# Kernel tuning notes

Measured on AMD Instinct MI355X. Metric: run time of the kernel, lower is better.

## Reference

```python
import jax, jax.numpy as jnp
import numpy as np

C = 256
C8 = C // 8

def setup_inputs() -> dict:
    key = jax.random.key(0)
    ks = jax.random.split(key, 8)
    a = jax.random.normal(ks[0], (4, C, 64, 64), dtype=jnp.float32)
    s = 1.0 / np.sqrt(C)
    b_w = jax.random.normal(ks[1], (C8, C), dtype=jnp.float32) * s
    b_b = jnp.zeros((C8,), dtype=jnp.float32)
    c_w = jax.random.normal(ks[2], (C8, C), dtype=jnp.float32) * s
    c_b = jnp.zeros((C8,), dtype=jnp.float32)
    d_w = jax.random.normal(ks[3], (C, C), dtype=jnp.float32) * s
    d_b = jnp.zeros((C,), dtype=jnp.float32)
    alpha = jnp.zeros((1,), dtype=jnp.float32) + 0.5  # nonzero so attention path is exercised
    return {"a": a, "b_w": b_w, "b_b": b_b, "c_w": c_w, "c_b": c_b, "d_w": d_w, "d_b": d_b, "alpha": alpha}

def _conv1x1(x, w, b):
    # x: [n, c, h, w], w: [o, c] -> [n, o, h, w]
    return jnp.einsum('nchw,oc->nohw', x, w) + b[None, :, None, None]

def reference(a, b_w, b_b, c_w, c_b, d_w, d_b, alpha):
    n, chan, h, w = a.shape
    nhw = h * w
    b = _conv1x1(a, b_w, b_b).reshape(n, -1, nhw)   # [n, C/8, nhw]
    c = _conv1x1(a, c_w, c_b).reshape(n, -1, nhw)   # [n, C/8, nhw]
    k = jnp.einsum('nci,ncj->nij', b, c)            # [n, nhw, nhw]
    s = jax.nn.softmax(k, axis=-1)
    d = _conv1x1(a, d_w, d_b).reshape(n, -1, nhw)   # [n, C, nhw]
    kl = jnp.einsum('ncj,nij->nci', d, s)           # d @ s^T
    kl = kl.reshape(n, chan, h, w)
    return alpha * kl + a
```

## Files before the change

kernel.cpp:

```cpp
#include <hip/hip_runtime.h>
#include <hip/hip_bf16.h>

#define CCH 256
#define CQK 32
#define NHW 4096

typedef float f32x4 __attribute__((ext_vector_type(4)));
typedef _Float16 hv8 __attribute__((ext_vector_type(8)));
typedef _Float16 hv4 __attribute__((ext_vector_type(4)));
typedef __fp16 fv2 __attribute__((ext_vector_type(2)));

__device__ __forceinline__ unsigned enc_f32(float f) {
    unsigned u = __float_as_uint(f);
    return (u & 0x80000000u) ? ~u : (u | 0x80000000u);
}
__device__ __forceinline__ float dec_f32(unsigned u) {
    return __uint_as_float((u & 0x80000000u) ? (u ^ 0x80000000u) : ~u);
}

__global__ __launch_bounds__(256) void prep_kernel(
    const float* __restrict__ b_w, const float* __restrict__ c_w,
    const float* __restrict__ d_w, _Float16* __restrict__ Wh,
    unsigned* __restrict__ m_enc)
{
    const int bid = blockIdx.x, tid = threadIdx.x;
    if (bid < 80) {
        const int idx = (bid * 256 + tid) * 4;
        const int row = idx >> 8, col = idx & 255;
        const float* src = (row < 32) ? (b_w + row * CCH + col)
                         : (row < 64) ? (c_w + (row - 32) * CCH + col)
                                      : (d_w + (row - 64) * CCH + col);
        const float scl = (row < 32) ? 1.4426950408889634f : 1.0f;
        float4 v = *reinterpret_cast<const float4*>(src);
        _Float16* dst = Wh + (size_t)row * CCH + col;
        dst[0] = (_Float16)(v.x * scl); dst[1] = (_Float16)(v.y * scl);
        dst[2] = (_Float16)(v.z * scl); dst[3] = (_Float16)(v.w * scl);
    } else {
        m_enc[(bid - 80) * 256 + tid] = 0u;
    }
}

__global__ __launch_bounds__(256) void proj_kernel(
    const float* __restrict__ a, const _Float16* __restrict__ Wh,
    const float* __restrict__ b_b, const float* __restrict__ c_b,
    const float* __restrict__ d_b,
    _Float16* __restrict__ bqT, _Float16* __restrict__ ckT,
    _Float16* __restrict__ dv)
{
    __shared__ _Float16 aT[32][CCH + 24];

    const int n    = blockIdx.x >> 7;
    const int i0   = (blockIdx.x & 127) << 5;
    const int tid  = threadIdx.x;
    const int lane = tid & 63;
    const int wave = tid >> 6;
    const int l15  = lane & 15;
    const int quad = lane >> 4;

    {
        const float* ap = a + (size_t)(n*CCH + tid)*NHW + i0;
        #pragma unroll
        for (int j = 0; j < 8; ++j) {
            float4 v = *reinterpret_cast<const float4*>(ap + j*4);
            aT[j*4+0][tid] = (_Float16)v.x;
            aT[j*4+1][tid] = (_Float16)v.y;
            aT[j*4+2][tid] = (_Float16)v.z;
            aT[j*4+3][tid] = (_Float16)v.w;
        }
    }
    __syncthreads();

    const f32x4 zf = {0.f, 0.f, 0.f, 0.f};
    f32x4 acc[5][2];
    #pragma unroll
    for (int t = 0; t < 5; ++t) { acc[t][0] = zf; acc[t][1] = zf; }

    const int ch0w = wave * 80;

    #pragma unroll
    for (int ks = 0; ks < 8; ++ks) {
        const int k0 = ks * 32;
        hv8 af0 = *reinterpret_cast<const hv8*>(&aT[l15][k0 + quad*8]);
        hv8 af1 = *reinterpret_cast<const hv8*>(&aT[16 + l15][k0 + quad*8]);
        #pragma unroll
        for (int t = 0; t < 5; ++t) {
            const int ch0 = ch0w + t*16;
            hv8 bf = *reinterpret_cast<const hv8*>(
                Wh + (size_t)(ch0 + l15)*CCH + k0 + quad*8);
            acc[t][0] = __builtin_amdgcn_mfma_f32_16x16x32_f16(af0, bf, acc[t][0], 0, 0, 0);
            acc[t][1] = __builtin_amdgcn_mfma_f32_16x16x32_f16(af1, bf, acc[t][1], 0, 0, 0);
        }
    }

    const int pos_b = i0 + quad*4;
    #pragma unroll
    for (int t = 0; t < 5; ++t) {
        const int ch0 = ch0w + t*16;
        if (ch0 < 64) {
            const float* bias_arr = (ch0 < 32) ? b_b : c_b;
            _Float16*    outp     = (ch0 < 32) ? bqT : ckT;
            const int    ch       = (ch0 & 31) + l15;
            const float  bias     = bias_arr[ch] *
                ((ch0 < 32) ? 1.4426950408889634f : 1.0f);
            #pragma unroll
            for (int nf = 0; nf < 2; ++nf) {
                #pragma unroll
                for (int r = 0; r < 4; ++r) {
                    const int pos = pos_b + nf*16 + r;
                    outp[((size_t)n*NHW + pos)*CQK + ch] =
                        (_Float16)(acc[t][nf][r] + bias);
                }
            }
        } else {
            const int ch   = ch0 - 64 + l15;
            const float bias = d_b[ch];
            #pragma unroll
            for (int nf = 0; nf < 2; ++nf) {
                hv4 v = { (_Float16)(acc[t][nf][0] + bias),
                          (_Float16)(acc[t][nf][1] + bias),
                          (_Float16)(acc[t][nf][2] + bias),
                          (_Float16)(acc[t][nf][3] + bias) };
                *reinterpret_cast<hv4*>(
                    dv + ((size_t)n*CCH + ch)*NHW + pos_b + nf*16) = v;
            }
        }
    }
}

__global__ __launch_bounds__(256) void rowmax_kernel(
    const _Float16* __restrict__ bqT, const _Float16* __restrict__ ckT,
    unsigned* __restrict__ m_enc)
{
    const int bx   = blockIdx.x;
    const int n    = bx >> 8;
    const int qt   = (bx >> 2) & 63;
    const int ks   = bx & 3;
    const int q0   = qt << 6;
    const int tid  = threadIdx.x;
    const int wave = tid >> 6;
    const int lane = tid & 63;
    const int l15  = lane & 15;
    const int quad = lane >> 4;

    const f32x4 zf = {0.f, 0.f, 0.f, 0.f};
    const hv8 qf = *reinterpret_cast<const hv8*>(
        bqT + ((size_t)n*NHW + q0 + wave*16 + l15)*CQK + quad*8);

    float mx = -1e30f;

    for (int kt = ks*16; kt < ks*16 + 16; ++kt) {
        const int k0 = kt << 6;
        #pragma unroll
        for (int f = 0; f < 4; ++f) {
            hv8 kf = *reinterpret_cast<const hv8*>(
                ckT + ((size_t)n*NHW + k0 + f*16 + l15)*CQK + quad*8);
            f32x4 s = __builtin_amdgcn_mfma_f32_16x16x32_f16(kf, qf, zf, 0, 0, 0);
            mx = fmaxf(mx, fmaxf(fmaxf(s[0], s[1]), fmaxf(s[2], s[3])));
        }
    }
    mx = fmaxf(mx, __shfl_xor(mx, 16, 64));
    mx = fmaxf(mx, __shfl_xor(mx, 32, 64));
    if (lane < 16)
        atomicMax(&m_enc[n*NHW + q0 + wave*16 + l15], enc_f32(mx));
}

__global__ __launch_bounds__(256) void attn_kernel(
    const _Float16* __restrict__ bqT, const _Float16* __restrict__ ckT,
    const _Float16* __restrict__ dv, const unsigned* __restrict__ m_enc,
    const float* __restrict__ a, const float* __restrict__ alpha_p,
    float* __restrict__ out)
{
    __shared__ _Float16 dv_lds[2][128 * 72];
    __shared__ _Float16 p_lds[2][4][16 * 72];

    const int bx   = ((blockIdx.x & 7) << 6) | (blockIdx.x >> 3);
    const int n    = bx >> 7;
    const int cg   = (bx >> 6) & 1;
    const int q0   = (bx & 63) << 6;
    const int co0  = cg << 7;
    const int tid  = threadIdx.x;
    const int wave = tid >> 6;
    const int lane = tid & 63;
    const int l15  = lane & 15;
    const int quad = lane >> 4;

    const _Float16 one_h = (_Float16)1.0f;
    const hv8 ones = { one_h, one_h, one_h, one_h, one_h, one_h, one_h, one_h };

    const hv8 qf = *reinterpret_cast<const hv8*>(
        bqT + ((size_t)n*NHW + q0 + wave*16 + l15)*CQK + quad*8);

    const float mneg = -dec_f32(m_enc[n*NHW + q0 + wave*16 + l15]);
    const f32x4 minit = {mneg, mneg, mneg, mneg};
    const f32x4 zf = {0.f, 0.f, 0.f, 0.f};

    f32x4 acc[8];
    #pragma unroll
    for (int t = 0; t < 8; ++t) acc[t] = zf;
    f32x4 acc_l = zf;

    const int co_s = tid >> 3;
    const int c8_s = (tid & 7) << 3;
    const _Float16* dvs0 = dv + ((size_t)(n*CCH + co0 + co_s))*NHW + c8_s;
    const _Float16* dvs1 = dvs0 + (size_t)32 * NHW;
    const _Float16* dvs2 = dvs0 + (size_t)64 * NHW;
    const _Float16* dvs3 = dvs0 + (size_t)96 * NHW;

    const _Float16* ckbase = ckT + ((size_t)n*NHW + l15)*CQK + quad*8;

    auto softmax_tile = [&](int buf, const hv8* kf) {
        #pragma unroll
        for (int f = 0; f < 4; ++f) {
            f32x4 s = __builtin_amdgcn_mfma_f32_16x16x32_f16(kf[f], qf, minit, 0, 0, 0);
            float p0 = __builtin_amdgcn_exp2f(s[0]);
            float p1 = __builtin_amdgcn_exp2f(s[1]);
            float p2 = __builtin_amdgcn_exp2f(s[2]);
            float p3 = __builtin_amdgcn_exp2f(s[3]);
            fv2 lo = __builtin_amdgcn_cvt_pkrtz(p0, p1);
            fv2 hi = __builtin_amdgcn_cvt_pkrtz(p2, p3);
            uint2 w;
            w.x = __builtin_bit_cast(unsigned, lo);
            w.y = __builtin_bit_cast(unsigned, hi);
            *reinterpret_cast<uint2*>(
                &p_lds[buf][wave][l15*72 + f*16 + quad*4]) = w;
        }
    };

    {
        int4 r0 = *reinterpret_cast<const int4*>(dvs0);
        int4 r1 = *reinterpret_cast<const int4*>(dvs1);
        int4 r2 = *reinterpret_cast<const int4*>(dvs2);
        int4 r3 = *reinterpret_cast<const int4*>(dvs3);
        *reinterpret_cast<int4*>(&dv_lds[0][co_s*72 + c8_s])        = r0;
        *reinterpret_cast<int4*>(&dv_lds[0][(co_s + 32)*72 + c8_s]) = r1;
        *reinterpret_cast<int4*>(&dv_lds[0][(co_s + 64)*72 + c8_s]) = r2;
        *reinterpret_cast<int4*>(&dv_lds[0][(co_s + 96)*72 + c8_s]) = r3;
        hv8 kf0[4];
        #pragma unroll
        for (int f = 0; f < 4; ++f)
            kf0[f] = *reinterpret_cast<const hv8*>(ckbase + (size_t)(f*16)*CQK);
        softmax_tile(0, kf0);
    }
    __syncthreads();

    for (int kt = 0; kt < 64; ++kt) {
        const int k0n = (kt + 1) << 6;
        const int cur = kt & 1;

        hv8 kfn[4];
        int4 nr0, nr1, nr2, nr3;
        if (kt < 63) {
            #pragma unroll
            for (int f = 0; f < 4; ++f)
                kfn[f] = *reinterpret_cast<const hv8*>(
                    ckbase + (size_t)(k0n + f*16)*CQK);
            nr0 = *reinterpret_cast<const int4*>(dvs0 + k0n);
            nr1 = *reinterpret_cast<const int4*>(dvs1 + k0n);
            nr2 = *reinterpret_cast<const int4*>(dvs2 + k0n);
            nr3 = *reinterpret_cast<const int4*>(dvs3 + k0n);
        }

        hv8 pf0 = *reinterpret_cast<const hv8*>(&p_lds[cur][wave][l15*72 + quad*8]);
        hv8 pf1 = *reinterpret_cast<const hv8*>(&p_lds[cur][wave][l15*72 + 32 + quad*8]);
        #pragma unroll
        for (int t = 0; t < 8; ++t) {
            hv8 d0 = *reinterpret_cast<const hv8*>(&dv_lds[cur][(t*16 + l15)*72 + quad*8]);
            acc[t] = __builtin_amdgcn_mfma_f32_16x16x32_f16(pf0, d0, acc[t], 0, 0, 0);
            hv8 d1 = *reinterpret_cast<const hv8*>(&dv_lds[cur][(t*16 + l15)*72 + 32 + quad*8]);
            acc[t] = __builtin_amdgcn_mfma_f32_16x16x32_f16(pf1, d1, acc[t], 0, 0, 0);
        }
        acc_l = __builtin_amdgcn_mfma_f32_16x16x32_f16(pf0, ones, acc_l, 0, 0, 0);
        acc_l = __builtin_amdgcn_mfma_f32_16x16x32_f16(pf1, ones, acc_l, 0, 0, 0);

        if (kt < 63) {
            softmax_tile(cur ^ 1, kfn);
            *reinterpret_cast<int4*>(&dv_lds[cur ^ 1][co_s*72 + c8_s])        = nr0;
            *reinterpret_cast<int4*>(&dv_lds[cur ^ 1][(co_s + 32)*72 + c8_s]) = nr1;
            *reinterpret_cast<int4*>(&dv_lds[cur ^ 1][(co_s + 64)*72 + c8_s]) = nr2;
            *reinterpret_cast<int4*>(&dv_lds[cur ^ 1][(co_s + 96)*72 + c8_s]) = nr3;
            __syncthreads();
        }
    }

    const float alpha = alpha_p[0];
    f32x4 rl;
    #pragma unroll
    for (int r = 0; r < 4; ++r) rl[r] = alpha / acc_l[r];

    const int qv = q0 + wave*16 + quad*4;
    #pragma unroll
    for (int t = 0; t < 8; ++t) {
        const int co = co0 + t*16 + l15;
        const size_t off = ((size_t)n*CCH + co)*NHW + qv;
        float4 av = *reinterpret_cast<const float4*>(a + off);
        float4 o;
        o.x = acc[t][0]*rl[0] + av.x;
        o.y = acc[t][1]*rl[1] + av.y;
        o.z = acc[t][2]*rl[2] + av.z;
        o.w = acc[t][3]*rl[3] + av.w;
        *reinterpret_cast<float4*>(out + off) = o;
    }
}

extern "C" void kernel_launch(void* const* d_in, const int* in_sizes, int n_in,
                              void* d_out, int out_size, void* d_ws, size_t ws_size,
                              hipStream_t stream)
{
    const float* a    = (const float*)d_in[0];
    const float* b_w  = (const float*)d_in[1];
    const float* b_b  = (const float*)d_in[2];
    const float* c_w  = (const float*)d_in[3];
    const float* c_b  = (const float*)d_in[4];
    const float* d_w  = (const float*)d_in[5];
    const float* d_b  = (const float*)d_in[6];
    const float* alp  = (const float*)d_in[7];
    float* out = (float*)d_out;

    _Float16* bqT  = (_Float16*)d_ws;
    _Float16* ckT  = bqT + (size_t)4*NHW*CQK;
    _Float16* dv   = ckT + (size_t)4*NHW*CQK;
    unsigned* m_enc = (unsigned*)(dv + (size_t)4*CCH*NHW);
    _Float16* Wh   = (_Float16*)(m_enc + 4*NHW);

    prep_kernel<<<144, 256, 0, stream>>>(b_w, c_w, d_w, Wh, m_enc);
    proj_kernel<<<512, 256, 0, stream>>>(a, Wh, b_b, c_b, d_b, bqT, ckT, dv);
    rowmax_kernel<<<1024, 256, 0, stream>>>(bqT, ckT, m_enc);
    attn_kernel<<<512, 256, 0, stream>>>(bqT, ckT, dv, m_enc, a, alp, out);
}
```

Baseline: 191.0 us.

## Retile attention blocks to 128 queries by 64 channels per block

Each attention block now covers 128 query positions and 64 output channels instead of 64 queries and 128 channels. Each wave computes two 16-query softmax groups against a shared 64-channel V tile. The aim is to halve global and LDS traffic for V per block and to reuse each V fragment across two MFMAs. The cost is that the QK^T MFMA and exp2 work for each query is now repeated in four channel-group blocks instead of two, and the P buffer is no longer double-buffered.

```diff
diff --git a/kernel.cpp b/kernel.cpp
--- a/kernel.cpp
+++ b/kernel.cpp
@@ -170,45 +170,50 @@
     const float* __restrict__ a, const float* __restrict__ alpha_p,
     float* __restrict__ out)
 {
-    __shared__ _Float16 dv_lds[2][128 * 72];
-    __shared__ _Float16 p_lds[2][4][16 * 72];
+    __shared__ __align__(16) _Float16 vlds[2][64 * 72];
+    __shared__ __align__(16) _Float16 p_lds[4][2][16 * 72];
 
     const int bx   = ((blockIdx.x & 7) << 6) | (blockIdx.x >> 3);
     const int n    = bx >> 7;
-    const int cg   = (bx >> 6) & 1;
-    const int q0   = (bx & 63) << 6;
-    const int co0  = cg << 7;
+    const int cg   = (bx >> 5) & 3;
+    const int qt   = bx & 31;
+    const int q0b  = qt << 7;
+    const int co0  = cg << 6;
     const int tid  = threadIdx.x;
     const int wave = tid >> 6;
     const int lane = tid & 63;
     const int l15  = lane & 15;
     const int quad = lane >> 4;
 
+    const f32x4 zf = {0.f, 0.f, 0.f, 0.f};
     const _Float16 one_h = (_Float16)1.0f;
     const hv8 ones = { one_h, one_h, one_h, one_h, one_h, one_h, one_h, one_h };
 
-    const hv8 qf = *reinterpret_cast<const hv8*>(
-        bqT + ((size_t)n*NHW + q0 + wave*16 + l15)*CQK + quad*8);
-
-    const float mneg = -dec_f32(m_enc[n*NHW + q0 + wave*16 + l15]);
-    const f32x4 minit = {mneg, mneg, mneg, mneg};
-    const f32x4 zf = {0.f, 0.f, 0.f, 0.f};
-
-    f32x4 acc[8];
-    #pragma unroll
-    for (int t = 0; t < 8; ++t) acc[t] = zf;
-    f32x4 acc_l = zf;
+    const int qA = q0b + wave*32 + l15;
+    const int qB = qA + 16;
+    const hv8 qfA = *reinterpret_cast<const hv8*>(
+        bqT + ((size_t)n*NHW + qA)*CQK + quad*8);
+    const hv8 qfB = *reinterpret_cast<const hv8*>(
+        bqT + ((size_t)n*NHW + qB)*CQK + quad*8);
+
+    const float mnegA = -dec_f32(m_enc[n*NHW + qA]);
+    const float mnegB = -dec_f32(m_enc[n*NHW + qB]);
+    const f32x4 minitA = {mnegA, mnegA, mnegA, mnegA};
+    const f32x4 minitB = {mnegB, mnegB, mnegB, mnegB};
+
+    f32x4 accA[4], accB[4];
+    #pragma unroll
+    for (int t = 0; t < 4; ++t) { accA[t] = zf; accB[t] = zf; }
+    f32x4 accLA = zf, accLB = zf;
 
     const int co_s = tid >> 3;
     const int c8_s = (tid & 7) << 3;
     const _Float16* dvs0 = dv + ((size_t)(n*CCH + co0 + co_s))*NHW + c8_s;
     const _Float16* dvs1 = dvs0 + (size_t)32 * NHW;
-    const _Float16* dvs2 = dvs0 + (size_t)64 * NHW;
-    const _Float16* dvs3 = dvs0 + (size_t)96 * NHW;
 
     const _Float16* ckbase = ckT + ((size_t)n*NHW + l15)*CQK + quad*8;
 
-    auto softmax_tile = [&](int buf, const hv8* kf) {
+    auto softmax_tile = [&](int grp, const hv8* kf, hv8 qf, f32x4 minit) {
         #pragma unroll
         for (int f = 0; f < 4; ++f) {
             f32x4 s = __builtin_amdgcn_mfma_f32_16x16x32_f16(kf[f], qf, minit, 0, 0, 0);
@@ -222,24 +227,21 @@
             w.x = __builtin_bit_cast(unsigned, lo);
             w.y = __builtin_bit_cast(unsigned, hi);
             *reinterpret_cast<uint2*>(
-                &p_lds[buf][wave][l15*72 + f*16 + quad*4]) = w;
+                &p_lds[wave][grp][l15*72 + f*16 + quad*4]) = w;
         }
     };
 
     {
         int4 r0 = *reinterpret_cast<const int4*>(dvs0);
         int4 r1 = *reinterpret_cast<const int4*>(dvs1);
-        int4 r2 = *reinterpret_cast<const int4*>(dvs2);
-        int4 r3 = *reinterpret_cast<const int4*>(dvs3);
-        *reinterpret_cast<int4*>(&dv_lds[0][co_s*72 + c8_s])        = r0;
-        *reinterpret_cast<int4*>(&dv_lds[0][(co_s + 32)*72 + c8_s]) = r1;
-        *reinterpret_cast<int4*>(&dv_lds[0][(co_s + 64)*72 + c8_s]) = r2;
-        *reinterpret_cast<int4*>(&dv_lds[0][(co_s + 96)*72 + c8_s]) = r3;
+        *reinterpret_cast<int4*>(&vlds[0][co_s*72 + c8_s])        = r0;
+        *reinterpret_cast<int4*>(&vlds[0][(co_s + 32)*72 + c8_s]) = r1;
         hv8 kf0[4];
         #pragma unroll
         for (int f = 0; f < 4; ++f)
             kf0[f] = *reinterpret_cast<const hv8*>(ckbase + (size_t)(f*16)*CQK);
-        softmax_tile(0, kf0);
+        softmax_tile(0, kf0, qfA, minitA);
+        softmax_tile(1, kf0, qfB, minitB);
     }
     __syncthreads();
 
@@ -248,7 +250,7 @@
         const int cur = kt & 1;
 
         hv8 kfn[4];
-        int4 nr0, nr1, nr2, nr3;
+        int4 nr0, nr1;
         if (kt < 63) {
             #pragma unroll
             for (int f = 0; f < 4; ++f)
@@ -256,49 +258,67 @@
                     ckbase + (size_t)(k0n + f*16)*CQK);
             nr0 = *reinterpret_cast<const int4*>(dvs0 + k0n);
             nr1 = *reinterpret_cast<const int4*>(dvs1 + k0n);
-            nr2 = *reinterpret_cast<const int4*>(dvs2 + k0n);
-            nr3 = *reinterpret_cast<const int4*>(dvs3 + k0n);
-        }
-
-        hv8 pf0 = *reinterpret_cast<const hv8*>(&p_lds[cur][wave][l15*72 + quad*8]);
-        hv8 pf1 = *reinterpret_cast<const hv8*>(&p_lds[cur][wave][l15*72 + 32 + quad*8]);
-        #pragma unroll
-        for (int t = 0; t < 8; ++t) {
-            hv8 d0 = *reinterpret_cast<const hv8*>(&dv_lds[cur][(t*16 + l15)*72 + quad*8]);
-            acc[t] = __builtin_amdgcn_mfma_f32_16x16x32_f16(pf0, d0, acc[t], 0, 0, 0);
-            hv8 d1 = *reinterpret_cast<const hv8*>(&dv_lds[cur][(t*16 + l15)*72 + 32 + quad*8]);
-            acc[t] = __builtin_amdgcn_mfma_f32_16x16x32_f16(pf1, d1, acc[t], 0, 0, 0);
-        }
-        acc_l = __builtin_amdgcn_mfma_f32_16x16x32_f16(pf0, ones, acc_l, 0, 0, 0);
-        acc_l = __builtin_amdgcn_mfma_f32_16x16x32_f16(pf1, ones, acc_l, 0, 0, 0);
+        }
+
+        hv8 pfA0 = *reinterpret_cast<const hv8*>(&p_lds[wave][0][l15*72 + quad*8]);
+        hv8 pfA1 = *reinterpret_cast<const hv8*>(&p_lds[wave][0][l15*72 + 32 + quad*8]);
+        hv8 pfB0 = *reinterpret_cast<const hv8*>(&p_lds[wave][1][l15*72 + quad*8]);
+        hv8 pfB1 = *reinterpret_cast<const hv8*>(&p_lds[wave][1][l15*72 + 32 + quad*8]);
+        #pragma unroll
+        for (int t = 0; t < 4; ++t) {
+            hv8 d0 = *reinterpret_cast<const hv8*>(&vlds[cur][(t*16 + l15)*72 + quad*8]);
+            accA[t] = __builtin_amdgcn_mfma_f32_16x16x32_f16(pfA0, d0, accA[t], 0, 0, 0);
+            accB[t] = __builtin_amdgcn_mfma_f32_16x16x32_f16(pfB0, d0, accB[t], 0, 0, 0);
+            hv8 d1 = *reinterpret_cast<const hv8*>(&vlds[cur][(t*16 + l15)*72 + 32 + quad*8]);
+            accA[t] = __builtin_amdgcn_mfma_f32_16x16x32_f16(pfA1, d1, accA[t], 0, 0, 0);
+            accB[t] = __builtin_amdgcn_mfma_f32_16x16x32_f16(pfB1, d1, accB[t], 0, 0, 0);
+        }
+        accLA = __builtin_amdgcn_mfma_f32_16x16x32_f16(pfA0, ones, accLA, 0, 0, 0);
+        accLA = __builtin_amdgcn_mfma_f32_16x16x32_f16(pfA1, ones, accLA, 0, 0, 0);
+        accLB = __builtin_amdgcn_mfma_f32_16x16x32_f16(pfB0, ones, accLB, 0, 0, 0);
+        accLB = __builtin_amdgcn_mfma_f32_16x16x32_f16(pfB1, ones, accLB, 0, 0, 0);
 
         if (kt < 63) {
-            softmax_tile(cur ^ 1, kfn);
-            *reinterpret_cast<int4*>(&dv_lds[cur ^ 1][co_s*72 + c8_s])        = nr0;
-            *reinterpret_cast<int4*>(&dv_lds[cur ^ 1][(co_s + 32)*72 + c8_s]) = nr1;
-            *reinterpret_cast<int4*>(&dv_lds[cur ^ 1][(co_s + 64)*72 + c8_s]) = nr2;
-            *reinterpret_cast<int4*>(&dv_lds[cur ^ 1][(co_s + 96)*72 + c8_s]) = nr3;
+            softmax_tile(0, kfn, qfA, minitA);
+            softmax_tile(1, kfn, qfB, minitB);
+            *reinterpret_cast<int4*>(&vlds[cur ^ 1][co_s*72 + c8_s])        = nr0;
+            *reinterpret_cast<int4*>(&vlds[cur ^ 1][(co_s + 32)*72 + c8_s]) = nr1;
             __syncthreads();
         }
     }
 
     const float alpha = alpha_p[0];
-    f32x4 rl;
-    #pragma unroll
-    for (int r = 0; r < 4; ++r) rl[r] = alpha / acc_l[r];
-
-    const int qv = q0 + wave*16 + quad*4;
-    #pragma unroll
-    for (int t = 0; t < 8; ++t) {
+    f32x4 rlA, rlB;
+    #pragma unroll
+    for (int r = 0; r < 4; ++r) {
+        rlA[r] = alpha / accLA[r];
+        rlB[r] = alpha / accLB[r];
+    }
+
+    const int qvA = q0b + wave*32 + quad*4;
+    #pragma unroll
+    for (int t = 0; t < 4; ++t) {
         const int co = co0 + t*16 + l15;
-        const size_t off = ((size_t)n*CCH + co)*NHW + qv;
-        float4 av = *reinterpret_cast<const float4*>(a + off);
-        float4 o;
-        o.x = acc[t][0]*rl[0] + av.x;
-        o.y = acc[t][1]*rl[1] + av.y;
-        o.z = acc[t][2]*rl[2] + av.z;
-        o.w = acc[t][3]*rl[3] + av.w;
-        *reinterpret_cast<float4*>(out + off) = o;
+        {
+            const size_t off = ((size_t)n*CCH + co)*NHW + qvA;
+            float4 av = *reinterpret_cast<const float4*>(a + off);
+            float4 o;
+            o.x = accA[t][0]*rlA[0] + av.x;
+            o.y = accA[t][1]*rlA[1] + av.y;
+            o.z = accA[t][2]*rlA[2] + av.z;
+            o.w = accA[t][3]*rlA[3] + av.w;
+            *reinterpret_cast<float4*>(out + off) = o;
+        }
+        {
+            const size_t off = ((size_t)n*CCH + co)*NHW + qvA + 16;
+            float4 av = *reinterpret_cast<const float4*>(a + off);
+            float4 o;
+            o.x = accB[t][0]*rlB[0] + av.x;
+            o.y = accB[t][1]*rlB[1] + av.y;
+            o.z = accB[t][2]*rlB[2] + av.z;
+            o.w = accB[t][3]*rlB[3] + av.w;
+            *reinterpret_cast<float4*>(out + off) = o;
+        }
     }
 }
 
```

Measured after the change: 193.3 us. Within noise of the previous version (+1.2%).

## Restructure attention kernel with split-K wave groups, larger query tiles, async LDS loads

Applied to the files above, without the earlier changes.

The attention kernel now uses 512-thread blocks covering 128 queries. The four wave groups each own a quarter of the key range (split-K), and their partial accumulators and row sums are reduced through LDS at the end. Each wave handles four 16-query sub-tiles, so every V fragment read from LDS feeds four MFMAs, and V tiles are staged with global_load_lds into an XOR-swizzled layout. This aims to raise data reuse and cut LDS and VGPR-staging traffic, at the cost of heavy register pressure from 128 accumulator floats per thread, a large LDS footprint, and an extra reduction epilogue.

```diff
diff --git a/kernel.cpp b/kernel.cpp
--- a/kernel.cpp
+++ b/kernel.cpp
@@ -16,6 +16,12 @@
 }
 __device__ __forceinline__ float dec_f32(unsigned u) {
     return __uint_as_float((u & 0x80000000u) ? (u ^ 0x80000000u) : ~u);
+}
+
+typedef __attribute__((address_space(3))) unsigned int lds_u32_t;
+typedef __attribute__((address_space(1))) const unsigned int glb_u32_t;
+__device__ __forceinline__ void gll16(const _Float16* gp, _Float16* lp) {
+    __builtin_amdgcn_global_load_lds((glb_u32_t*)gp, (lds_u32_t*)lp, 16, 0, 0);
 }
 
 __global__ __launch_bounds__(256) void prep_kernel(
@@ -164,141 +170,230 @@
         atomicMax(&m_enc[n*NHW + q0 + wave*16 + l15], enc_f32(mx));
 }
 
-__global__ __launch_bounds__(256) void attn_kernel(
+__global__ __launch_bounds__(512, 2) void attn_kernel(
     const _Float16* __restrict__ bqT, const _Float16* __restrict__ ckT,
     const _Float16* __restrict__ dv, const unsigned* __restrict__ m_enc,
     const float* __restrict__ a, const float* __restrict__ alpha_p,
     float* __restrict__ out)
 {
-    __shared__ _Float16 dv_lds[2][128 * 72];
-    __shared__ _Float16 p_lds[2][4][16 * 72];
-
-    const int bx   = ((blockIdx.x & 7) << 6) | (blockIdx.x >> 3);
-    const int n    = bx >> 7;
-    const int cg   = (bx >> 6) & 1;
-    const int q0   = (bx & 63) << 6;
+    __shared__ __align__(16) char smem[141312];
+
+    const int bx   = ((blockIdx.x & 7) << 5) | (blockIdx.x >> 3);
+    const int n    = bx >> 6;
+    const int cg   = (bx >> 5) & 1;
+    const int qt   = bx & 31;
+    const int q0b  = qt << 7;
     const int co0  = cg << 7;
     const int tid  = threadIdx.x;
     const int wave = tid >> 6;
+    const int g    = wave >> 1;
+    const int qw   = wave & 1;
     const int lane = tid & 63;
     const int l15  = lane & 15;
     const int quad = lane >> 4;
-
+    const int kg0  = g << 10;
+
+    _Float16* vbuf = (_Float16*)(smem + (g << 14));
+    _Float16* pb   = (_Float16*)(smem + 65536 + wave*9216);
+    float*    lbuf = (float*)(smem + 139264);
+
+    const f32x4 zf = {0.f, 0.f, 0.f, 0.f};
     const _Float16 one_h = (_Float16)1.0f;
     const hv8 ones = { one_h, one_h, one_h, one_h, one_h, one_h, one_h, one_h };
 
-    const hv8 qf = *reinterpret_cast<const hv8*>(
-        bqT + ((size_t)n*NHW + q0 + wave*16 + l15)*CQK + quad*8);
-
-    const float mneg = -dec_f32(m_enc[n*NHW + q0 + wave*16 + l15]);
-    const f32x4 minit = {mneg, mneg, mneg, mneg};
-    const f32x4 zf = {0.f, 0.f, 0.f, 0.f};
-
-    f32x4 acc[8];
-    #pragma unroll
-    for (int t = 0; t < 8; ++t) acc[t] = zf;
-    f32x4 acc_l = zf;
-
-    const int co_s = tid >> 3;
-    const int c8_s = (tid & 7) << 3;
-    const _Float16* dvs0 = dv + ((size_t)(n*CCH + co0 + co_s))*NHW + c8_s;
-    const _Float16* dvs1 = dvs0 + (size_t)32 * NHW;
-    const _Float16* dvs2 = dvs0 + (size_t)64 * NHW;
-    const _Float16* dvs3 = dvs0 + (size_t)96 * NHW;
-
-    const _Float16* ckbase = ckT + ((size_t)n*NHW + l15)*CQK + quad*8;
-
-    auto softmax_tile = [&](int buf, const hv8* kf) {
-        #pragma unroll
-        for (int f = 0; f < 4; ++f) {
-            f32x4 s = __builtin_amdgcn_mfma_f32_16x16x32_f16(kf[f], qf, minit, 0, 0, 0);
-            float p0 = __builtin_amdgcn_exp2f(s[0]);
-            float p1 = __builtin_amdgcn_exp2f(s[1]);
-            float p2 = __builtin_amdgcn_exp2f(s[2]);
-            float p3 = __builtin_amdgcn_exp2f(s[3]);
-            fv2 lo = __builtin_amdgcn_cvt_pkrtz(p0, p1);
-            fv2 hi = __builtin_amdgcn_cvt_pkrtz(p2, p3);
-            uint2 w;
-            w.x = __builtin_bit_cast(unsigned, lo);
-            w.y = __builtin_bit_cast(unsigned, hi);
-            *reinterpret_cast<uint2*>(
-                &p_lds[buf][wave][l15*72 + f*16 + quad*4]) = w;
+    hv8 qf[4]; float mneg[4];
+    #pragma unroll
+    for (int X = 0; X < 4; ++X) {
+        const int q = q0b + qw*64 + X*16 + l15;
+        qf[X] = *reinterpret_cast<const hv8*>(
+            bqT + ((size_t)n*NHW + q)*CQK + quad*8);
+        mneg[X] = -dec_f32(m_enc[n*NHW + q]);
+    }
+
+    f32x4 acc[4][8];
+    #pragma unroll
+    for (int X = 0; X < 4; ++X)
+        #pragma unroll
+        for (int t = 0; t < 8; ++t) acc[X][t] = zf;
+    f32x4 accL[4];
+    #pragma unroll
+    for (int X = 0; X < 4; ++X) accL[X] = zf;
+
+    const int rl8 = lane >> 3;
+    const _Float16* dvs = dv
+        + (size_t)(n*CCH + co0 + qw*64 + rl8)*NHW + kg0 + 8*((lane & 7) ^ rl8);
+    _Float16* ldsb = (_Float16*)(smem + (g << 14) + qw*8192);
+
+    const _Float16* ckbase = ckT + ((size_t)(n*NHW + kg0 + l15))*CQK + quad*8;
+
+    const int c0h = ((quad*16) ^ ((l15 & 7) << 4)) >> 1;
+    const int c1h = ((64 + quad*16) ^ ((l15 & 7) << 4)) >> 1;
+
+    auto softmax_tile = [&](const hv8* kf) {
+        #pragma unroll
+        for (int X = 0; X < 4; ++X) {
+            const f32x4 minit = {mneg[X], mneg[X], mneg[X], mneg[X]};
+            #pragma unroll
+            for (int f = 0; f < 4; ++f) {
+                f32x4 s = __builtin_amdgcn_mfma_f32_16x16x32_f16(
+                    kf[f], qf[X], minit, 0, 0, 0);
+                float p0 = __builtin_amdgcn_exp2f(s[0]);
+                float p1 = __builtin_amdgcn_exp2f(s[1]);
+                float p2 = __builtin_amdgcn_exp2f(s[2]);
+                float p3 = __builtin_amdgcn_exp2f(s[3]);
+                fv2 lo = __builtin_amdgcn_cvt_pkrtz(p0, p1);
+                fv2 hi = __builtin_amdgcn_cvt_pkrtz(p2, p3);
+                uint2 w;
+                w.x = __builtin_bit_cast(unsigned, lo);
+                w.y = __builtin_bit_cast(unsigned, hi);
+                *reinterpret_cast<uint2*>(
+                    pb + X*1152 + l15*72 + f*16 + quad*4) = w;
+            }
         }
     };
 
+    hv8 pf0[4], pf1[4];
+    auto read_pf = [&]() {
+        #pragma unroll
+        for (int X = 0; X < 4; ++X) {
+            pf0[X] = *reinterpret_cast<const hv8*>(pb + X*1152 + l15*72 + quad*8);
+            pf1[X] = *reinterpret_cast<const hv8*>(pb + X*1152 + l15*72 + 32 + quad*8);
+        }
+    };
+
+    auto stage = [&](int kt) {
+        #pragma unroll
+        for (int j = 0; j < 8; ++j)
+            gll16(dvs + (size_t)(j*8)*NHW + kt*64, ldsb + (size_t)(j*8)*64);
+    };
+
+    auto load_kf = [&](int key0, hv8* kf) {
+        #pragma unroll
+        for (int f = 0; f < 4; ++f)
+            kf[f] = *reinterpret_cast<const hv8*>(
+                ckbase + (size_t)(key0 + f*16)*CQK);
+    };
+
     {
-        int4 r0 = *reinterpret_cast<const int4*>(dvs0);
-        int4 r1 = *reinterpret_cast<const int4*>(dvs1);
-        int4 r2 = *reinterpret_cast<const int4*>(dvs2);
-        int4 r3 = *reinterpret_cast<const int4*>(dvs3);
-        *reinterpret_cast<int4*>(&dv_lds[0][co_s*72 + c8_s])        = r0;
-        *reinterpret_cast<int4*>(&dv_lds[0][(co_s + 32)*72 + c8_s]) = r1;
-        *reinterpret_cast<int4*>(&dv_lds[0][(co_s + 64)*72 + c8_s]) = r2;
-        *reinterpret_cast<int4*>(&dv_lds[0][(co_s + 96)*72 + c8_s]) = r3;
+        stage(0);
         hv8 kf0[4];
-        #pragma unroll
-        for (int f = 0; f < 4; ++f)
-            kf0[f] = *reinterpret_cast<const hv8*>(ckbase + (size_t)(f*16)*CQK);
-        softmax_tile(0, kf0);
-    }
-    __syncthreads();
-
-    for (int kt = 0; kt < 64; ++kt) {
-        const int k0n = (kt + 1) << 6;
-        const int cur = kt & 1;
-
+        load_kf(0, kf0);
+        softmax_tile(kf0);
+        read_pf();
+    }
+    __syncthreads();
+
+    for (int kt = 0; kt < 16; ++kt) {
         hv8 kfn[4];
-        int4 nr0, nr1, nr2, nr3;
-        if (kt < 63) {
-            #pragma unroll
-            for (int f = 0; f < 4; ++f)
-                kfn[f] = *reinterpret_cast<const hv8*>(
-                    ckbase + (size_t)(k0n + f*16)*CQK);
-            nr0 = *reinterpret_cast<const int4*>(dvs0 + k0n);
-            nr1 = *reinterpret_cast<const int4*>(dvs1 + k0n);
-            nr2 = *reinterpret_cast<const int4*>(dvs2 + k0n);
-            nr3 = *reinterpret_cast<const int4*>(dvs3 + k0n);
-        }
-
-        hv8 pf0 = *reinterpret_cast<const hv8*>(&p_lds[cur][wave][l15*72 + quad*8]);
-        hv8 pf1 = *reinterpret_cast<const hv8*>(&p_lds[cur][wave][l15*72 + 32 + quad*8]);
+        if (kt < 15) load_kf((kt + 1)*64, kfn);
+
         #pragma unroll
         for (int t = 0; t < 8; ++t) {
-            hv8 d0 = *reinterpret_cast<const hv8*>(&dv_lds[cur][(t*16 + l15)*72 + quad*8]);
-            acc[t] = __builtin_amdgcn_mfma_f32_16x16x32_f16(pf0, d0, acc[t], 0, 0, 0);
-            hv8 d1 = *reinterpret_cast<const hv8*>(&dv_lds[cur][(t*16 + l15)*72 + 32 + quad*8]);
-            acc[t] = __builtin_amdgcn_mfma_f32_16x16x32_f16(pf1, d1, acc[t], 0, 0, 0);
-        }
-        acc_l = __builtin_amdgcn_mfma_f32_16x16x32_f16(pf0, ones, acc_l, 0, 0, 0);
-        acc_l = __builtin_amdgcn_mfma_f32_16x16x32_f16(pf1, ones, acc_l, 0, 0, 0);
-
-        if (kt < 63) {
-            softmax_tile(cur ^ 1, kfn);
-            *reinterpret_cast<int4*>(&dv_lds[cur ^ 1][co_s*72 + c8_s])        = nr0;
-            *reinterpret_cast<int4*>(&dv_lds[cur ^ 1][(co_s + 32)*72 + c8_s]) = nr1;
-            *reinterpret_cast<int4*>(&dv_lds[cur ^ 1][(co_s + 64)*72 + c8_s]) = nr2;
-            *reinterpret_cast<int4*>(&dv_lds[cur ^ 1][(co_s + 96)*72 + c8_s]) = nr3;
+            const _Float16* vr = vbuf + (t*16 + l15)*64;
+            hv8 d0 = *reinterpret_cast<const hv8*>(vr + c0h);
+            #pragma unroll
+            for (int X = 0; X < 4; ++X)
+                acc[X][t] = __builtin_amdgcn_mfma_f32_16x16x32_f16(
+                    pf0[X], d0, acc[X][t], 0, 0, 0);
+            hv8 d1 = *reinterpret_cast<const hv8*>(vr + c1h);
+            #pragma unroll
+            for (int X = 0; X < 4; ++X)
+                acc[X][t] = __builtin_amdgcn_mfma_f32_16x16x32_f16(
+                    pf1[X], d1, acc[X][t], 0, 0, 0);
+        }
+        #pragma unroll
+        for (int X = 0; X < 4; ++X) {
+            accL[X] = __builtin_amdgcn_mfma_f32_16x16x32_f16(pf0[X], ones, accL[X], 0, 0, 0);
+            accL[X] = __builtin_amdgcn_mfma_f32_16x16x32_f16(pf1[X], ones, accL[X], 0, 0, 0);
+        }
+
+        if (kt < 15) {
+            softmax_tile(kfn);
             __syncthreads();
-        }
-    }
-
-    const float alpha = alpha_p[0];
-    f32x4 rl;
-    #pragma unroll
-    for (int r = 0; r < 4; ++r) rl[r] = alpha / acc_l[r];
-
-    const int qv = q0 + wave*16 + quad*4;
-    #pragma unroll
-    for (int t = 0; t < 8; ++t) {
-        const int co = co0 + t*16 + l15;
-        const size_t off = ((size_t)n*CCH + co)*NHW + qv;
-        float4 av = *reinterpret_cast<const float4*>(a + off);
-        float4 o;
-        o.x = acc[t][0]*rl[0] + av.x;
-        o.y = acc[t][1]*rl[1] + av.y;
-        o.z = acc[t][2]*rl[2] + av.z;
-        o.w = acc[t][3]*rl[3] + av.w;
-        *reinterpret_cast<float4*>(out + off) = o;
+            stage(kt + 1);
+            read_pf();
+            __syncthreads();
+        }
+    }
+
+    __syncthreads();
+    float* buf1 = (float*)smem;
+    float* buf2 = (float*)(smem + 67584);
+
+    if (l15 == 0) {
+        #pragma unroll
+        for (int X = 0; X < 4; ++X)
+            *reinterpret_cast<float4*>(&lbuf[g*128 + qw*64 + X*16 + quad*4]) =
+                *reinterpret_cast<float4*>(&accL[X]);
+    }
+    if (g == 1 || g == 3) {
+        float* b = (g == 1) ? buf1 : buf2;
+        #pragma unroll
+        for (int X = 0; X < 4; ++X)
+            #pragma unroll
+            for (int t = 0; t < 8; ++t)
+                *reinterpret_cast<float4*>(
+                    &b[(t*16 + l15)*132 + qw*64 + X*16 + quad*4]) =
+                    *reinterpret_cast<float4*>(&acc[X][t]);
+    }
+    __syncthreads();
+    if (g == 0 || g == 2) {
+        float* b = (g == 0) ? buf1 : buf2;
+        #pragma unroll
+        for (int X = 0; X < 4; ++X)
+            #pragma unroll
+            for (int t = 0; t < 8; ++t) {
+                float4 p = *reinterpret_cast<float4*>(
+                    &b[(t*16 + l15)*132 + qw*64 + X*16 + quad*4]);
+                acc[X][t][0] += p.x; acc[X][t][1] += p.y;
+                acc[X][t][2] += p.z; acc[X][t][3] += p.w;
+            }
+    }
+    __syncthreads();
+    if (g == 2) {
+        #pragma unroll
+        for (int X = 0; X < 4; ++X)
+            #pragma unroll
+            for (int t = 0; t < 8; ++t)
+                *reinterpret_cast<float4*>(
+                    &buf1[(t*16 + l15)*132 + qw*64 + X*16 + quad*4]) =
+                    *reinterpret_cast<float4*>(&acc[X][t]);
+    }
+    __syncthreads();
+    if (g == 0) {
+        const float alpha = alpha_p[0];
+        #pragma unroll
+        for (int X = 0; X < 4; ++X) {
+            const int qloc = qw*64 + X*16 + quad*4;
+            #pragma unroll
+            for (int t = 0; t < 8; ++t) {
+                float4 p = *reinterpret_cast<float4*>(
+                    &buf1[(t*16 + l15)*132 + qloc]);
+                acc[X][t][0] += p.x; acc[X][t][1] += p.y;
+                acc[X][t][2] += p.z; acc[X][t][3] += p.w;
+            }
+            float4 l0 = *reinterpret_cast<float4*>(&lbuf[0*128 + qloc]);
+            float4 l1 = *reinterpret_cast<float4*>(&lbuf[1*128 + qloc]);
+            float4 l2 = *reinterpret_cast<float4*>(&lbuf[2*128 + qloc]);
+            float4 l3 = *reinterpret_cast<float4*>(&lbuf[3*128 + qloc]);
+            f32x4 rl;
+            rl[0] = alpha / (l0.x + l1.x + l2.x + l3.x);
+            rl[1] = alpha / (l0.y + l1.y + l2.y + l3.y);
+            rl[2] = alpha / (l0.z + l1.z + l2.z + l3.z);
+            rl[3] = alpha / (l0.w + l1.w + l2.w + l3.w);
+            #pragma unroll
+            for (int t = 0; t < 8; ++t) {
+                const size_t off =
+                    ((size_t)(n*CCH + co0 + t*16 + l15))*NHW + q0b + qloc;
+                float4 av = *reinterpret_cast<const float4*>(a + off);
+                float4 o;
+                o.x = acc[X][t][0]*rl[0] + av.x;
+                o.y = acc[X][t][1]*rl[1] + av.y;
+                o.z = acc[X][t][2]*rl[2] + av.z;
+                o.w = acc[X][t][3]*rl[3] + av.w;
+                *reinterpret_cast<float4*>(out + off) = o;
+            }
+        }
     }
 }
 
@@ -325,5 +420,5 @@
     prep_kernel<<<144, 256, 0, stream>>>(b_w, c_w, d_w, Wh, m_enc);
     proj_kernel<<<512, 256, 0, stream>>>(a, Wh, b_b, c_b, d_b, bqT, ckT, dv);
     rowmax_kernel<<<1024, 256, 0, stream>>>(bqT, ckT, m_enc);
-    attn_kernel<<<512, 256, 0, stream>>>(bqT, ckT, dv, m_enc, a, alp, out);
-}
+    attn_kernel<<<256, 512, 0, stream>>>(bqT, ckT, dv, m_enc, a, alp, out);
+}
```

Result: faster. 175.7 us (-8.0%).
